# Kernel optimization log

Hardware: AMD Instinct MI355X
Metric: run time of the kernel (lower is better)

The kernel has to match this reference:

```python
import jax, jax.numpy as jnp
import numpy as np

D_MODEL = 1024
ED = 2048          # d_inner = 2 * d_model
N = 16             # d_state
DT_RANK = 64
K = 4              # d_conv
BETA = 0.6
ALPHA = 1.0
B_SZ, L = 1, 2048


def setup_inputs() -> dict:
    key = jax.random.key(0)
    ks = jax.random.split(key, 9)
    s = 0.02
    x = jax.random.normal(ks[0], (B_SZ, L, D_MODEL), jnp.float32)
    W_in = jax.random.normal(ks[1], (2 * ED, D_MODEL), jnp.float32) * s
    conv_w = jax.random.normal(ks[2], (ED, K), jnp.float32) * s
    conv_b = jax.random.normal(ks[3], (ED,), jnp.float32) * s
    W_x = jax.random.normal(ks[4], (DT_RANK + 2 * N, ED), jnp.float32) * s
    dt_std = DT_RANK ** -0.5
    W_dt = jax.random.uniform(ks[5], (ED, DT_RANK), jnp.float32, -dt_std, dt_std)
    # dt bias init: inverse-softplus of dt in [dt_min, dt_max]
    dt = jnp.exp(jax.random.uniform(ks[6], (ED,), jnp.float32)
                 * (np.log(0.1) - np.log(0.001)) + np.log(0.001))
    dt = jnp.clip(dt, 1e-4)
    b_dt = dt + jnp.log(-jnp.expm1(-dt))
    A_log = jnp.log(jnp.tile(jnp.arange(1, N + 1, dtype=jnp.float32), (ED, 1)))
    D = jnp.ones((ED,), jnp.float32)
    W_out = jax.random.normal(ks[7], (D_MODEL, ED), jnp.float32) * s
    return {"x": x, "W_in": W_in, "conv_w": conv_w, "conv_b": conv_b,
            "W_x": W_x, "W_dt": W_dt, "b_dt": b_dt, "A_log": A_log,
            "D": D, "W_out": W_out}


def _depthwise_causal_conv(xc, conv_w, conv_b):
    # xc: (B, L, ED); torch Conv1d(groups=ED, padding=K-1)[..., :L] == causal conv
    lhs = jnp.transpose(xc, (0, 2, 1))                       # (B, ED, L)
    lhs = jnp.pad(lhs, ((0, 0), (0, 0), (K - 1, 0)))
    out = jax.lax.conv_general_dilated(lhs, conv_w[:, None, :], (1,), 'VALID',
                                       feature_group_count=ED)  # (B, ED, L)
    return jnp.transpose(out, (0, 2, 1)) + conv_b


def _ssm_momentum(xc, W_x, W_dt, b_dt, A_log, D):
    A = -jnp.exp(A_log)                                      # (ED, N)
    dBC = xc @ W_x.T                                         # (B, L, dt_rank + 2N)
    delta, Bm, Cm = jnp.split(dBC, [DT_RANK, DT_RANK + N], axis=-1)
    delta = jax.nn.softplus(delta @ W_dt.T + b_dt)           # (B, L, ED)
    deltaA = jnp.exp(delta[..., None] * A)                   # (B, L, ED, N)
    u = ALPHA * delta[..., None] * Bm[:, :, None, :] * xc[..., None]  # (B, L, ED, N)

    def step(carry, inp):
        h, v = carry
        dA_t, u_t = inp
        v = BETA * v + u_t
        h = dA_t * h + v
        return (h, v), h

    h0 = jnp.zeros((xc.shape[0], ED, N), xc.dtype)
    _, hs = jax.lax.scan(step, (h0, h0),
                         (jnp.moveaxis(deltaA, 1, 0), jnp.moveaxis(u, 1, 0)))
    y = jnp.einsum('lben,bln->ble', hs, Cm)                  # (B, L, ED)
    return y + D * xc


def reference(x, W_in, conv_w, conv_b, W_x, W_dt, b_dt, A_log, D, W_out):
    xz = x @ W_in.T                                          # (B, L, 2*ED)
    xc, z = jnp.split(xz, 2, axis=-1)
    xc = jax.nn.silu(_depthwise_causal_conv(xc, conv_w, conv_b))
    y = _ssm_momentum(xc, W_x, W_dt, b_dt, A_log, D)
    return (y * jax.nn.silu(z)) @ W_out.T                    # (B, L, d_model)
```

## Files before the change

### kernel.cpp

```cpp
#include <hip/hip_runtime.h>
#include <hip/hip_bf16.h>
#include <math.h>

#define L 2048
#define DM 1024
#define ED 2048
#define NST 16
#define DTR 64
#define BETA 0.6f
#define NCHUNK 64
#define LCH 32
#define SPLITS 16
#define SPLIT4 4

typedef __bf16 bf16_t;
typedef __bf16 bf16x8 __attribute__((ext_vector_type(8)));
typedef __bf16 bf16x4 __attribute__((ext_vector_type(4)));
typedef float  floatx4 __attribute__((ext_vector_type(4)));


__global__ void k_fill(float* __restrict__ p, float v, int n) {
    int i = blockIdx.x * 256 + threadIdx.x;
    if (i < n) p[i] = v;
}

__global__ void k_cvt4(const float4* __restrict__ src, bf16x4* __restrict__ dst, int n4) {
    int i = blockIdx.x * 256 + threadIdx.x;
    if (i < n4) {
        float4 f = src[i];
        bf16x4 o;
        o[0] = (bf16_t)f.x; o[1] = (bf16_t)f.y; o[2] = (bf16_t)f.z; o[3] = (bf16_t)f.w;
        dst[i] = o;
    }
}

template<int EPI, bool GUARD>
__global__ __launch_bounds__(256)
void k_gemm_bt(const bf16_t* __restrict__ X, const bf16_t* __restrict__ W,
               float* __restrict__ C, int M, int N, int K, int ldc, int ksz,
               const float* __restrict__ bias) {
    __shared__ bf16_t As[128 * 32];
    __shared__ bf16_t Bs[128 * 32];
    const int tid  = threadIdx.x;
    const int bx   = blockIdx.x, by = blockIdx.y;
    const int kbase = blockIdx.z * ksz;
    C += (size_t)blockIdx.z * M * ldc;
    const int wave = tid >> 6, lane = tid & 63;
    const int wm   = (wave >> 1) * 64;
    const int wn   = (wave & 1) * 64;
    const int quad = lane >> 4, l16 = lane & 15;

    floatx4 acc[4][4];
#pragma unroll
    for (int i = 0; i < 4; i++)
#pragma unroll
        for (int j = 0; j < 4; j++)
            acc[i][j] = (floatx4){0.f, 0.f, 0.f, 0.f};

    for (int kt = kbase; kt < kbase + ksz; kt += 32) {
        if (GUARD) {
#pragma unroll
            for (int p = 0; p < 2; p++) {
                int e = p * 2048 + tid * 8;
                int r = e >> 5, c = e & 31;
                int arow = by * 128 + r;
                *(float4*)(&As[r * 32 + c]) =
                    *(const float4*)(&X[(size_t)arow * K + kt + c]);
                int brow = bx * 128 + r;
                float4 bv = make_float4(0.f, 0.f, 0.f, 0.f);
                if (brow < N) bv = *(const float4*)(&W[(size_t)brow * K + kt + c]);
                *(float4*)(&Bs[r * 32 + c]) = bv;
            }
        } else {
#pragma unroll
            for (int p = 0; p < 2; p++) {
                int e = p * 2048 + tid * 8;
                int r = e >> 5, c = e & 31;
                __builtin_amdgcn_global_load_lds(
                    (const __attribute__((address_space(1))) void*)&X[(size_t)(by * 128 + r) * K + kt + c],
                    (__attribute__((address_space(3))) void*)&As[e], 16, 0, 0);
                __builtin_amdgcn_global_load_lds(
                    (const __attribute__((address_space(1))) void*)&W[(size_t)(bx * 128 + r) * K + kt + c],
                    (__attribute__((address_space(3))) void*)&Bs[e], 16, 0, 0);
            }
        }
        __syncthreads();

        bf16x8 af[4], bfr[4];
#pragma unroll
        for (int mt = 0; mt < 4; mt++)
            af[mt] = *(const bf16x8*)(&As[(wm + mt * 16 + l16) * 32 + quad * 8]);
#pragma unroll
        for (int nt = 0; nt < 4; nt++)
            bfr[nt] = *(const bf16x8*)(&Bs[(wn + nt * 16 + l16) * 32 + quad * 8]);
#pragma unroll
        for (int mt = 0; mt < 4; mt++)
#pragma unroll
            for (int nt = 0; nt < 4; nt++)
                acc[mt][nt] = __builtin_amdgcn_mfma_f32_16x16x32_bf16(
                    af[mt], bfr[nt], acc[mt][nt], 0, 0, 0);
        __syncthreads();
    }

#pragma unroll
    for (int mt = 0; mt < 4; mt++) {
#pragma unroll
        for (int nt = 0; nt < 4; nt++) {
            int col = bx * 128 + wn + nt * 16 + l16;
            if (!GUARD || col < N) {
#pragma unroll
                for (int r4 = 0; r4 < 4; r4++) {
                    int row = by * 128 + wm + mt * 16 + quad * 4 + r4;
                    float v = acc[mt][nt][r4];
                    if (EPI == 1) {
                        v += bias[col];
                        v = (v > 20.f) ? v : log1pf(__expf(v));
                    }
                    C[(size_t)row * ldc + col] = v;
                }
            }
        }
    }
}

__global__ void k_red4(const float4* __restrict__ part, float4* __restrict__ out) {
    int i = blockIdx.x * 256 + threadIdx.x;
    const int stride = L * DM / 4;
    float4 a = part[i], b = part[i + stride];
    float4 c = part[i + 2 * stride], d = part[i + 3 * stride];
    out[i] = make_float4(a.x + b.x + c.x + d.x, a.y + b.y + c.y + d.y,
                         a.z + b.z + c.z + d.z, a.w + b.w + c.w + d.w);
}

__global__ void k_conv_silu(const float* __restrict__ xz,
                            const float* __restrict__ conv_w,
                            const float* __restrict__ conv_b,
                            float* __restrict__ xc, bf16_t* __restrict__ xc_bf) {
    int idx = blockIdx.x * 256 + threadIdx.x;
    int e = idx & (ED - 1);
    int t = idx >> 11;
    float w0 = conv_w[e * 4 + 0], w1 = conv_w[e * 4 + 1];
    float w2 = conv_w[e * 4 + 2], w3 = conv_w[e * 4 + 3];
    const float* col = xz + e;
    float acc = conv_b[e];
    if (t >= 3) acc += w0 * col[(size_t)(t - 3) * 4096];
    if (t >= 2) acc += w1 * col[(size_t)(t - 2) * 4096];
    if (t >= 1) acc += w2 * col[(size_t)(t - 1) * 4096];
    acc += w3 * col[(size_t)t * 4096];
    float s = acc / (1.f + __expf(-acc));
    xc[idx] = s;
    xc_bf[idx] = (bf16_t)s;
}

__global__ void k_red2(const float* __restrict__ part, float* __restrict__ dBC,
                       bf16_t* __restrict__ dly) {
    int idx = blockIdx.x * 256 + threadIdx.x;
    int t = idx / 96, c = idx - t * 96;
    float s = 0.f;
#pragma unroll
    for (int sp = 0; sp < SPLITS; sp++) s += part[(size_t)sp * L * 96 + idx];
    dBC[idx] = s;
    if (c < 64) dly[t * 64 + c] = (bf16_t)s;
}


__global__ __launch_bounds__(256)
void k_scan_p1(const float* __restrict__ delta, const float* __restrict__ xc,
               const float* __restrict__ dBC, const float* __restrict__ A_log,
               float4* __restrict__ summ) {
    const int chunk = blockIdx.x >> 3;
    const int e = (blockIdx.x & 7) * 256 + threadIdx.x;
    float A[NST];
#pragma unroll
    for (int n = 0; n < NST; n++) A[n] = -__expf(A_log[e * NST + n]);
    float h[NST], v[NST], p[NST], q[NST];
#pragma unroll
    for (int n = 0; n < NST; n++) { h[n] = 0.f; v[n] = 0.f; p[n] = 1.f; q[n] = 0.f; }
    float bp = 1.f;
    const int t0 = chunk * LCH;
    for (int i = 0; i < LCH; i++) {
        int t = t0 + i;
        float d   = delta[(size_t)t * ED + e];
        float xcv = xc[(size_t)t * ED + e];
        float du  = d * xcv;
        bp *= BETA;
        const float* Bp = &dBC[t * 96 + 64];
#pragma unroll
        for (int n = 0; n < NST; n++) {
            float a = __expf(d * A[n]);
            v[n] = BETA * v[n] + du * Bp[n];
            h[n] = a * h[n] + v[n];
            p[n] *= a;
            q[n] = a * q[n] + bp;
        }
    }
#pragma unroll
    for (int n = 0; n < NST; n++)
        summ[((size_t)n * NCHUNK + chunk) * ED + e] = make_float4(h[n], v[n], p[n], q[n]);
}

__global__ void k_combine(float4* __restrict__ summ) {
    int tid = blockIdx.x * 256 + threadIdx.x;
    int n = tid >> 11, e = tid & (ED - 1);
    float2* s2 = (float2*)summ;
    float h = 0.f, v = 0.f;
    const float bl = 7.9586611e-8f;
#pragma unroll 4
    for (int c = 0; c < NCHUNK; c++) {
        size_t idx = ((size_t)n * NCHUNK + c) * ED + e;
        float4 f = summ[idx];
        s2[idx * 2] = make_float2(h, v);
        float hn = f.z * h + f.w * v + f.x;
        v = bl * v + f.y;
        h = hn;
    }
}

__global__ __launch_bounds__(256)
void k_scan_p2(const float* __restrict__ delta, const float* __restrict__ xc,
               const float* __restrict__ dBC, const float* __restrict__ A_log,
               const float4* __restrict__ summ, const float* __restrict__ Dvec,
               const float* __restrict__ xz, bf16_t* __restrict__ g) {
    const int chunk = blockIdx.x >> 3;
    const int e = (blockIdx.x & 7) * 256 + threadIdx.x;
    float A[NST];
#pragma unroll
    for (int n = 0; n < NST; n++) A[n] = -__expf(A_log[e * NST + n]);
    float h[NST], v[NST];
    const float2* s2 = (const float2*)summ;
#pragma unroll
    for (int n = 0; n < NST; n++) {
        float2 s = s2[(((size_t)n * NCHUNK + chunk) * ED + e) * 2];
        h[n] = s.x; v[n] = s.y;
    }
    const float De = Dvec[e];
    const int t0 = chunk * LCH;
    for (int i = 0; i < LCH; i++) {
        int t = t0 + i;
        float d   = delta[(size_t)t * ED + e];
        float xcv = xc[(size_t)t * ED + e];
        float du  = d * xcv;
        const float* Bp = &dBC[t * 96 + 64];
        const float* Cp = &dBC[t * 96 + 80];
        float yacc = 0.f;
#pragma unroll
        for (int n = 0; n < NST; n++) {
            float a = __expf(d * A[n]);
            v[n] = BETA * v[n] + du * Bp[n];
            h[n] = a * h[n] + v[n];
            yacc += Cp[n] * h[n];
        }
        float z = xz[(size_t)t * 4096 + ED + e];
        float sz = z / (1.f + __expf(-z));
        g[(size_t)t * ED + e] = (bf16_t)((yacc + De * xcv) * sz);
    }
}


extern "C" void kernel_launch(void* const* d_in, const int* in_sizes, int n_in,
                              void* d_out, int out_size, void* d_ws, size_t ws_size,
                              hipStream_t stream) {
    const float* x      = (const float*)d_in[0];
    const float* W_in   = (const float*)d_in[1];
    const float* conv_w = (const float*)d_in[2];
    const float* conv_b = (const float*)d_in[3];
    const float* W_x    = (const float*)d_in[4];
    const float* W_dt   = (const float*)d_in[5];
    const float* b_dt   = (const float*)d_in[6];
    const float* A_log  = (const float*)d_in[7];
    const float* Dv     = (const float*)d_in[8];
    const float* W_out  = (const float*)d_in[9];
    float* out = (float*)d_out;

    constexpr size_t OFF_XZ    = 0;
    constexpr size_t OFF_XC    = 33554432;
    constexpr size_t OFF_C     = 50331648;
    constexpr size_t OFF_DELTA = 58720256;
    constexpr size_t OFF_R1    = 75497472;
    constexpr size_t OFF_XBF   = 109051904;
    constexpr size_t OFF_DBC   = 113246208;
    constexpr size_t OFF_DLY   = 114032640;
    constexpr size_t OFF_WX    = 114294784;
    constexpr size_t OFF_WDT   = 114688000;
    constexpr size_t OFF_WOUT  = 114950144;
    constexpr size_t WS_NEED   = 119144448;

    if (ws_size < WS_NEED) {
        k_fill<<<(out_size + 255) / 256, 256, 0, stream>>>(out, 1.0e9f, out_size);
        return;
    }

    char* ws = (char*)d_ws;
    float*  xz    = (float*)(ws + OFF_XZ);
    float*  part4 = (float*)(ws + OFF_XZ);
    float*  xc    = (float*)(ws + OFF_XC);
    bf16_t* xc_bf = (bf16_t*)(ws + OFF_C);
    bf16_t* g_bf  = (bf16_t*)(ws + OFF_C);
    float*  delta = (float*)(ws + OFF_DELTA);
    bf16_t* Win_bf  = (bf16_t*)(ws + OFF_R1);
    float*  part2   = (float*)(ws + OFF_R1 + 16777216);
    float4* summ    = (float4*)(ws + OFF_R1);
    bf16_t* x_bf  = (bf16_t*)(ws + OFF_XBF);
    float*  dBC   = (float*)(ws + OFF_DBC);
    bf16_t* dly   = (bf16_t*)(ws + OFF_DLY);
    bf16_t* Wx_bf  = (bf16_t*)(ws + OFF_WX);
    bf16_t* Wdt_bf = (bf16_t*)(ws + OFF_WDT);
    bf16_t* Wout_bf = (bf16_t*)(ws + OFF_WOUT);

    auto cvt = [&](const float* s, bf16_t* d, int n) {
        k_cvt4<<<(n / 4 + 255) / 256, 256, 0, stream>>>((const float4*)s, (bf16x4*)d, n / 4);
    };

    cvt(x, x_bf, L * DM);
    cvt(W_in, Win_bf, 2 * ED * DM);
    cvt(W_x, Wx_bf, 96 * ED);
    cvt(W_dt, Wdt_bf, ED * DTR);
    cvt(W_out, Wout_bf, DM * ED);

    {
        dim3 g(4096 / 128, L / 128, 1);
        k_gemm_bt<0, false><<<g, 256, 0, stream>>>(x_bf, Win_bf, xz, L, 4096, DM, 4096, DM, nullptr);
    }
    k_conv_silu<<<L * ED / 256, 256, 0, stream>>>(xz, conv_w, conv_b, xc, xc_bf);
    {
        dim3 g(1, L / 128, SPLITS);
        k_gemm_bt<0, true><<<g, 256, 0, stream>>>(xc_bf, Wx_bf, part2, L, 96, ED, 96, ED / SPLITS, nullptr);
    }
    k_red2<<<L * 96 / 256, 256, 0, stream>>>(part2, dBC, dly);
    {
        dim3 g(ED / 128, L / 128, 1);
        k_gemm_bt<1, false><<<g, 256, 0, stream>>>(dly, Wdt_bf, delta, L, ED, DTR, ED, DTR, b_dt);
    }
    k_scan_p1<<<NCHUNK * 8, 256, 0, stream>>>(delta, xc, dBC, A_log, summ);
    k_combine<<<ED * NST / 256, 256, 0, stream>>>(summ);
    k_scan_p2<<<NCHUNK * 8, 256, 0, stream>>>(delta, xc, dBC, A_log, summ, Dv, xz, g_bf);
    {
        dim3 g(DM / 128, L / 128, SPLIT4);
        k_gemm_bt<0, false><<<g, 256, 0, stream>>>(g_bf, Wout_bf, part4, L, DM, ED, DM, ED / SPLIT4, nullptr);
    }
    k_red4<<<L * DM / 4 / 256, 256, 0, stream>>>((const float4*)part4, (float4*)out);
}
```

Before: 278.2 us.

## Store intermediates in bf16 and fuse weight conversions into one launch

Intermediate tensors that used to be fp32 (xz, delta, xc, the split-K partials of the output GEMM) are now written and read as bf16. The GEMM epilogue gains a bf16 store mode, and the scan and conv kernels convert on load. The five fp32-to-bf16 conversion launches become a single kernel. The aim is to cut memory traffic and launch overhead in these bandwidth-bound stages, at the cost of lower precision in delta and in the partial sums before the final reduction.

```diff
diff --git a/kernel.cpp b/kernel.cpp
--- a/kernel.cpp
+++ b/kernel.cpp
@@ -24,14 +24,22 @@
     if (i < n) p[i] = v;
 }
 
-__global__ void k_cvt4(const float4* __restrict__ src, bf16x4* __restrict__ dst, int n4) {
+__global__ void k_cvt_all(const float4* __restrict__ s0, bf16x4* __restrict__ d0,
+                          const float4* __restrict__ s1, bf16x4* __restrict__ d1,
+                          const float4* __restrict__ s2, bf16x4* __restrict__ d2,
+                          const float4* __restrict__ s3, bf16x4* __restrict__ d3,
+                          const float4* __restrict__ s4, bf16x4* __restrict__ d4) {
     int i = blockIdx.x * 256 + threadIdx.x;
-    if (i < n4) {
-        float4 f = src[i];
-        bf16x4 o;
-        o[0] = (bf16_t)f.x; o[1] = (bf16_t)f.y; o[2] = (bf16_t)f.z; o[3] = (bf16_t)f.w;
-        dst[i] = o;
-    }
+    const float4* s; bf16x4* d; int j;
+    if (i < 524288)        { s = s0; d = d0; j = i; }
+    else if (i < 1572864)  { s = s1; d = d1; j = i - 524288; }
+    else if (i < 1622016)  { s = s2; d = d2; j = i - 1572864; }
+    else if (i < 1654784)  { s = s3; d = d3; j = i - 1622016; }
+    else                   { s = s4; d = d4; j = i - 1654784; }
+    float4 f = s[j];
+    bf16x4 o;
+    o[0] = (bf16_t)f.x; o[1] = (bf16_t)f.y; o[2] = (bf16_t)f.z; o[3] = (bf16_t)f.w;
+    d[j] = o;
 }
 
 template<int EPI, bool GUARD>
@@ -44,7 +52,7 @@
     const int tid  = threadIdx.x;
     const int bx   = blockIdx.x, by = blockIdx.y;
     const int kbase = blockIdx.z * ksz;
-    C += (size_t)blockIdx.z * M * ldc;
+    const size_t zoff = (size_t)blockIdx.z * M * ldc;
     const int wave = tid >> 6, lane = tid & 63;
     const int wm   = (wave >> 1) * 64;
     const int wn   = (wave & 1) * 64;
@@ -112,43 +120,56 @@
                 for (int r4 = 0; r4 < 4; r4++) {
                     int row = by * 128 + wm + mt * 16 + quad * 4 + r4;
                     float v = acc[mt][nt][r4];
-                    if (EPI == 1) {
+                    size_t off = zoff + (size_t)row * ldc + col;
+                    if (EPI == 0) {
+                        C[off] = v;
+                    } else if (EPI == 1) {
                         v += bias[col];
                         v = (v > 20.f) ? v : log1pf(__expf(v));
+                        ((bf16_t*)C)[off] = (bf16_t)v;
+                    } else {
+                        ((bf16_t*)C)[off] = (bf16_t)v;
                     }
-                    C[(size_t)row * ldc + col] = v;
                 }
             }
         }
     }
 }
 
-__global__ void k_red4(const float4* __restrict__ part, float4* __restrict__ out) {
+__global__ void k_red4(const bf16x8* __restrict__ part, float4* __restrict__ out) {
     int i = blockIdx.x * 256 + threadIdx.x;
-    const int stride = L * DM / 4;
-    float4 a = part[i], b = part[i + stride];
-    float4 c = part[i + 2 * stride], d = part[i + 3 * stride];
-    out[i] = make_float4(a.x + b.x + c.x + d.x, a.y + b.y + c.y + d.y,
-                         a.z + b.z + c.z + d.z, a.w + b.w + c.w + d.w);
-}
-
-__global__ void k_conv_silu(const float* __restrict__ xz,
+    const int stride = L * DM / 8;
+    bf16x8 a = part[i], b = part[i + stride];
+    bf16x8 c = part[i + 2 * stride], d = part[i + 3 * stride];
+    float4 o0, o1;
+    o0.x = (float)a[0] + (float)b[0] + (float)c[0] + (float)d[0];
+    o0.y = (float)a[1] + (float)b[1] + (float)c[1] + (float)d[1];
+    o0.z = (float)a[2] + (float)b[2] + (float)c[2] + (float)d[2];
+    o0.w = (float)a[3] + (float)b[3] + (float)c[3] + (float)d[3];
+    o1.x = (float)a[4] + (float)b[4] + (float)c[4] + (float)d[4];
+    o1.y = (float)a[5] + (float)b[5] + (float)c[5] + (float)d[5];
+    o1.z = (float)a[6] + (float)b[6] + (float)c[6] + (float)d[6];
+    o1.w = (float)a[7] + (float)b[7] + (float)c[7] + (float)d[7];
+    out[2 * i]     = o0;
+    out[2 * i + 1] = o1;
+}
+
+__global__ void k_conv_silu(const bf16_t* __restrict__ xz,
                             const float* __restrict__ conv_w,
                             const float* __restrict__ conv_b,
-                            float* __restrict__ xc, bf16_t* __restrict__ xc_bf) {
+                            bf16_t* __restrict__ xc_bf) {
     int idx = blockIdx.x * 256 + threadIdx.x;
     int e = idx & (ED - 1);
     int t = idx >> 11;
     float w0 = conv_w[e * 4 + 0], w1 = conv_w[e * 4 + 1];
     float w2 = conv_w[e * 4 + 2], w3 = conv_w[e * 4 + 3];
-    const float* col = xz + e;
+    const bf16_t* col = xz + e;
     float acc = conv_b[e];
-    if (t >= 3) acc += w0 * col[(size_t)(t - 3) * 4096];
-    if (t >= 2) acc += w1 * col[(size_t)(t - 2) * 4096];
-    if (t >= 1) acc += w2 * col[(size_t)(t - 1) * 4096];
-    acc += w3 * col[(size_t)t * 4096];
+    if (t >= 3) acc += w0 * (float)col[(size_t)(t - 3) * 4096];
+    if (t >= 2) acc += w1 * (float)col[(size_t)(t - 2) * 4096];
+    if (t >= 1) acc += w2 * (float)col[(size_t)(t - 1) * 4096];
+    acc += w3 * (float)col[(size_t)t * 4096];
     float s = acc / (1.f + __expf(-acc));
-    xc[idx] = s;
     xc_bf[idx] = (bf16_t)s;
 }
 
@@ -165,7 +186,7 @@
 
 
 __global__ __launch_bounds__(256)
-void k_scan_p1(const float* __restrict__ delta, const float* __restrict__ xc,
+void k_scan_p1(const bf16_t* __restrict__ delta, const bf16_t* __restrict__ xc,
                const float* __restrict__ dBC, const float* __restrict__ A_log,
                float4* __restrict__ summ) {
     const int chunk = blockIdx.x >> 3;
@@ -180,8 +201,8 @@
     const int t0 = chunk * LCH;
     for (int i = 0; i < LCH; i++) {
         int t = t0 + i;
-        float d   = delta[(size_t)t * ED + e];
-        float xcv = xc[(size_t)t * ED + e];
+        float d   = (float)delta[(size_t)t * ED + e];
+        float xcv = (float)xc[(size_t)t * ED + e];
         float du  = d * xcv;
         bp *= BETA;
         const float* Bp = &dBC[t * 96 + 64];
@@ -199,17 +220,16 @@
         summ[((size_t)n * NCHUNK + chunk) * ED + e] = make_float4(h[n], v[n], p[n], q[n]);
 }
 
-__global__ void k_combine(float4* __restrict__ summ) {
+__global__ void k_combine(const float4* __restrict__ summ, float2* __restrict__ inc) {
     int tid = blockIdx.x * 256 + threadIdx.x;
     int n = tid >> 11, e = tid & (ED - 1);
-    float2* s2 = (float2*)summ;
     float h = 0.f, v = 0.f;
     const float bl = 7.9586611e-8f;
 #pragma unroll 4
     for (int c = 0; c < NCHUNK; c++) {
         size_t idx = ((size_t)n * NCHUNK + c) * ED + e;
         float4 f = summ[idx];
-        s2[idx * 2] = make_float2(h, v);
+        inc[idx] = make_float2(h, v);
         float hn = f.z * h + f.w * v + f.x;
         v = bl * v + f.y;
         h = hn;
@@ -217,28 +237,27 @@
 }
 
 __global__ __launch_bounds__(256)
-void k_scan_p2(const float* __restrict__ delta, const float* __restrict__ xc,
+void k_scan_p2(const bf16_t* __restrict__ delta, const bf16_t* __restrict__ xc,
                const float* __restrict__ dBC, const float* __restrict__ A_log,
-               const float4* __restrict__ summ, const float* __restrict__ Dvec,
-               const float* __restrict__ xz, bf16_t* __restrict__ g) {
+               const float2* __restrict__ inc, const float* __restrict__ Dvec,
+               const bf16_t* __restrict__ xz, bf16_t* __restrict__ g) {
     const int chunk = blockIdx.x >> 3;
     const int e = (blockIdx.x & 7) * 256 + threadIdx.x;
     float A[NST];
 #pragma unroll
     for (int n = 0; n < NST; n++) A[n] = -__expf(A_log[e * NST + n]);
     float h[NST], v[NST];
-    const float2* s2 = (const float2*)summ;
 #pragma unroll
     for (int n = 0; n < NST; n++) {
-        float2 s = s2[(((size_t)n * NCHUNK + chunk) * ED + e) * 2];
+        float2 s = inc[((size_t)n * NCHUNK + chunk) * ED + e];
         h[n] = s.x; v[n] = s.y;
     }
     const float De = Dvec[e];
     const int t0 = chunk * LCH;
     for (int i = 0; i < LCH; i++) {
         int t = t0 + i;
-        float d   = delta[(size_t)t * ED + e];
-        float xcv = xc[(size_t)t * ED + e];
+        float d   = (float)delta[(size_t)t * ED + e];
+        float xcv = (float)xc[(size_t)t * ED + e];
         float du  = d * xcv;
         const float* Bp = &dBC[t * 96 + 64];
         const float* Cp = &dBC[t * 96 + 80];
@@ -250,7 +269,7 @@
             h[n] = a * h[n] + v[n];
             yacc += Cp[n] * h[n];
         }
-        float z = xz[(size_t)t * 4096 + ED + e];
+        float z = (float)xz[(size_t)t * 4096 + ED + e];
         float sz = z / (1.f + __expf(-z));
         g[(size_t)t * ED + e] = (bf16_t)((yacc + De * xcv) * sz);
     }
@@ -291,12 +310,12 @@
     }
 
     char* ws = (char*)d_ws;
-    float*  xz    = (float*)(ws + OFF_XZ);
-    float*  part4 = (float*)(ws + OFF_XZ);
-    float*  xc    = (float*)(ws + OFF_XC);
+    bf16_t* xz_bf = (bf16_t*)(ws + OFF_XZ);
+    bf16_t* part4 = (bf16_t*)(ws + OFF_XZ);
+    float2* inc   = (float2*)(ws + OFF_XC);
     bf16_t* xc_bf = (bf16_t*)(ws + OFF_C);
-    bf16_t* g_bf  = (bf16_t*)(ws + OFF_C);
-    float*  delta = (float*)(ws + OFF_DELTA);
+    bf16_t* delta_bf = (bf16_t*)(ws + OFF_DELTA);
+    bf16_t* g_bf  = (bf16_t*)(ws + OFF_DELTA + 8388608);
     bf16_t* Win_bf  = (bf16_t*)(ws + OFF_R1);
     float*  part2   = (float*)(ws + OFF_R1 + 16777216);
     float4* summ    = (float4*)(ws + OFF_R1);
@@ -307,21 +326,18 @@
     bf16_t* Wdt_bf = (bf16_t*)(ws + OFF_WDT);
     bf16_t* Wout_bf = (bf16_t*)(ws + OFF_WOUT);
 
-    auto cvt = [&](const float* s, bf16_t* d, int n) {
-        k_cvt4<<<(n / 4 + 255) / 256, 256, 0, stream>>>((const float4*)s, (bf16x4*)d, n / 4);
-    };
-
-    cvt(x, x_bf, L * DM);
-    cvt(W_in, Win_bf, 2 * ED * DM);
-    cvt(W_x, Wx_bf, 96 * ED);
-    cvt(W_dt, Wdt_bf, ED * DTR);
-    cvt(W_out, Wout_bf, DM * ED);
+    k_cvt_all<<<8512, 256, 0, stream>>>(
+        (const float4*)x,     (bf16x4*)x_bf,
+        (const float4*)W_in,  (bf16x4*)Win_bf,
+        (const float4*)W_x,   (bf16x4*)Wx_bf,
+        (const float4*)W_dt,  (bf16x4*)Wdt_bf,
+        (const float4*)W_out, (bf16x4*)Wout_bf);
 
     {
         dim3 g(4096 / 128, L / 128, 1);
-        k_gemm_bt<0, false><<<g, 256, 0, stream>>>(x_bf, Win_bf, xz, L, 4096, DM, 4096, DM, nullptr);
-    }
-    k_conv_silu<<<L * ED / 256, 256, 0, stream>>>(xz, conv_w, conv_b, xc, xc_bf);
+        k_gemm_bt<2, false><<<g, 256, 0, stream>>>(x_bf, Win_bf, (float*)xz_bf, L, 4096, DM, 4096, DM, nullptr);
+    }
+    k_conv_silu<<<L * ED / 256, 256, 0, stream>>>(xz_bf, conv_w, conv_b, xc_bf);
     {
         dim3 g(1, L / 128, SPLITS);
         k_gemm_bt<0, true><<<g, 256, 0, stream>>>(xc_bf, Wx_bf, part2, L, 96, ED, 96, ED / SPLITS, nullptr);
@@ -329,14 +345,14 @@
     k_red2<<<L * 96 / 256, 256, 0, stream>>>(part2, dBC, dly);
     {
         dim3 g(ED / 128, L / 128, 1);
-        k_gemm_bt<1, false><<<g, 256, 0, stream>>>(dly, Wdt_bf, delta, L, ED, DTR, ED, DTR, b_dt);
-    }
-    k_scan_p1<<<NCHUNK * 8, 256, 0, stream>>>(delta, xc, dBC, A_log, summ);
-    k_combine<<<ED * NST / 256, 256, 0, stream>>>(summ);
-    k_scan_p2<<<NCHUNK * 8, 256, 0, stream>>>(delta, xc, dBC, A_log, summ, Dv, xz, g_bf);
+        k_gemm_bt<1, false><<<g, 256, 0, stream>>>(dly, Wdt_bf, (float*)delta_bf, L, ED, DTR, ED, DTR, b_dt);
+    }
+    k_scan_p1<<<NCHUNK * 8, 256, 0, stream>>>(delta_bf, xc_bf, dBC, A_log, summ);
+    k_combine<<<ED * NST / 256, 256, 0, stream>>>(summ, inc);
+    k_scan_p2<<<NCHUNK * 8, 256, 0, stream>>>(delta_bf, xc_bf, dBC, A_log, inc, Dv, xz_bf, g_bf);
     {
         dim3 g(DM / 128, L / 128, SPLIT4);
-        k_gemm_bt<0, false><<<g, 256, 0, stream>>>(g_bf, Wout_bf, part4, L, DM, ED, DM, ED / SPLIT4, nullptr);
-    }
-    k_red4<<<L * DM / 4 / 256, 256, 0, stream>>>((const float4*)part4, (float4*)out);
-}
+        k_gemm_bt<2, false><<<g, 256, 0, stream>>>(g_bf, Wout_bf, (float*)part4, L, DM, ED, DM, ED / SPLIT4, nullptr);
+    }
+    k_red4<<<L * DM / 8 / 256, 256, 0, stream>>>((const bf16x8*)part4, (float4*)out);
+}
```

Result: slower. 305.8 us (+9.9%).
